# Performance work log

Measured on AMD Instinct MI355X. Metric: run time of the kernel, lower is better.

The kernel has to match this reference:

```python
import jax, jax.numpy as jnp
import numpy as np

COMMITMENT_COST = 0.25


def setup_inputs() -> dict:
    key = jax.random.key(0)
    k1, k2 = jax.random.split(key)
    inputs = jax.random.normal(k1, (32, 64, 64, 64), dtype=jnp.float32)  # b c h w
    num_embeddings, embedding_dim = 1024, 64
    # matches torch uniform_(-1/K, 1/K) init distributionally
    embedding = jax.random.uniform(
        k2, (num_embeddings, embedding_dim), dtype=jnp.float32,
        minval=-1.0 / num_embeddings, maxval=1.0 / num_embeddings)
    return {"inputs": inputs, "embedding": embedding}


def reference(inputs, embedding):
    # b c h w -> b h w c
    x = jnp.transpose(inputs, (0, 2, 3, 1))
    b, h, w, c = x.shape
    flat = x.reshape(-1, c)  # [N, D]
    dists = (jnp.sum(flat * flat, axis=1, keepdims=True)
             + jnp.sum(embedding * embedding, axis=1)
             - 2.0 * flat @ embedding.T)  # [N, K]
    idx = jnp.argmin(dists, axis=1)  # [N]
    quantized = embedding[idx].reshape(b, h, w, c)  # gather == one-hot matmul
    # elementwise MSE losses (reduction='none'); stop-gradient mirrors .detach()
    e_latent = (jax.lax.stop_gradient(quantized) - x) ** 2
    q_latent = (quantized - jax.lax.stop_gradient(x)) ** 2
    loss = q_latent + COMMITMENT_COST * e_latent  # [b, h, w, c]
    # straight-through estimator
    quantized_st = x + jax.lax.stop_gradient(quantized - x)
    quantized_out = jnp.transpose(quantized_st, (0, 3, 1, 2))  # b h w c -> b c h w
    return quantized_out, loss, idx.reshape(b, h, w)
```

## Files before the change

kernel.cpp:

```cpp
#include <hip/hip_runtime.h>

#define NPTS    131072
#define KC      1024
#define DD      64
#define HWSZ    4096
#define MARGINF 6e-5f
#define SLACKF  4e-5f

typedef __attribute__((ext_vector_type(8))) short short8;
typedef __attribute__((ext_vector_type(4))) float f32x4;

__device__ __forceinline__ ushort bf16_rne(float x) {
    unsigned u = __float_as_uint(x);
    unsigned r = u + 0x7fffu + ((u >> 16) & 1u);
    return (ushort)(r >> 16);
}

__device__ __forceinline__ float rdlane(float v, int d) {
    return __int_as_float(__builtin_amdgcn_readlane(__float_as_int(v), d));
}

__device__ __forceinline__ float exact_dv(float xrv, const float* __restrict__ emb,
                                          const float* __restrict__ se32,
                                          float sx, int k) {
    const float* er = emb + k * DD;
    double a = 0.0;
#pragma unroll 4
    for (int d = 0; d < DD; ++d)
        a = fma((double)rdlane(xrv, d), (double)er[d], a);
    float mm = (float)(2.0 * a);
    float s1, Dv;
    {
#pragma clang fp contract(off)
        s1 = sx + se32[k];
        Dv = s1 - mm;
    }
    return Dv;
}

__global__ void __launch_bounds__(256)
vq_prep_e(const float* __restrict__ emb, float* __restrict__ se32,
          float* __restrict__ sebB, ushort* __restrict__ Ebuf,
          float* __restrict__ embT, int* __restrict__ cnt) {
    __shared__ float es[16][68];
    const int tid  = threadIdx.x;
    const int tile = blockIdx.x;
    const int kbase = tile * 16;

    if (tile == 0 && tid == 0) *cnt = 0;

#pragma unroll
    for (int it = 0; it < 4; ++it) {
        int f = it * 256 + tid;
        es[f >> 6][f & 63] = emb[(size_t)kbase * DD + f];
    }
    __syncthreads();

    if (tid < 16) {
        float rr[8];
#pragma unroll
        for (int di = 0; di < 8; ++di) rr[di] = 0.0f;
        {
#pragma clang fp contract(off)
#pragma unroll
            for (int dm = 0; dm < 8; ++dm)
#pragma unroll
                for (int di = 0; di < 8; ++di) {
                    float ev = es[tid][dm * 8 + di];
                    rr[di] += ev * ev;
                }
        }
        float s;
        {
#pragma clang fp contract(off)
            s = ((rr[0] + rr[1]) + (rr[2] + rr[3])) + ((rr[4] + rr[5]) + (rr[6] + rr[7]));
        }
        se32[kbase + tid] = s;
        sebB[kbase + tid] = s + 0.5f;
    }

#pragma unroll
    for (int it = 0; it < 4; ++it) {
        int f = it * 256 + tid;
        int d = f >> 4, colk = f & 15;
        embT[d * KC + kbase + colk] = es[colk][d];
    }

#pragma unroll
    for (int it = 0; it < 8; ++it) {
        int f = it * 256 + tid;
        int sub = f >> 9;
        int pos = f & 511;
        int kh = sub >> 1, hl = sub & 1;
        int jj = pos & 7, colk = (pos >> 3) & 15, quad = pos >> 7;
        float ev = es[colk][kh * 32 + quad * 8 + jj];
        ushort hb = bf16_rne(ev);
        ushort val;
        if (hl == 0) {
            val = hb;
        } else {
            float hf = __uint_as_float(((unsigned)hb) << 16);
            val = bf16_rne(ev - hf);
        }
        Ebuf[((tile * 2 + kh) * 2 + hl) * 512 + pos] = val;
    }
}

__global__ void __launch_bounds__(256)
vq_main(const float* __restrict__ in, const float* __restrict__ emb,
        const ushort* __restrict__ Ebuf, const float* __restrict__ sebB,
        float* __restrict__ outq, float* __restrict__ outl, float* __restrict__ outi,
        int* __restrict__ cnt, int* __restrict__ queue) {
    __shared__ float xs[64][129];
    __shared__ int   sidx[128];
    const int tid = threadIdx.x;
    const int n0  = blockIdx.x * 128;
    const int b   = n0 >> 12;
    const int hw0 = n0 & 4095;
    const float* inb = in + (size_t)b * DD * HWSZ;

#pragma unroll
    for (int it = 0; it < 32; ++it) {
        int f = tid + it * 256;
        int c = f >> 7, j = f & 127;
        xs[c][j] = inb[c * HWSZ + hw0 + j];
    }
    __syncthreads();

    const int lane = tid & 63, wave = tid >> 6;
    const int quad = lane >> 4, col = lane & 15;

    short8 A[2][2][2];
#pragma unroll
    for (int p = 0; p < 2; ++p) {
        int pt = wave * 32 + p * 16 + col;
#pragma unroll
        for (int kh = 0; kh < 2; ++kh) {
            short8 ah, al;
#pragma unroll
            for (int j = 0; j < 8; ++j) {
                float xv = xs[kh * 32 + quad * 8 + j][pt];
                ushort hb = bf16_rne(xv);
                float  hf = __uint_as_float(((unsigned)hb) << 16);
                ah[j] = (short)hb;
                al[j] = (short)bf16_rne(xv - hf);
            }
            A[p][kh][0] = ah; A[p][kh][1] = al;
        }
    }

    unsigned b1[8], b2[8];
#pragma unroll
    for (int s = 0; s < 8; ++s) { b1[s] = 0xFFFFFFFFu; b2[s] = 0xFFFFFFFFu; }

    for (int g = 0; g < 16; ++g) {
        short8 B[4][2][2];
        float  sB[4];
#pragma unroll
        for (int s = 0; s < 4; ++s) {
            int tile = g * 4 + s;
            sB[s] = sebB[tile * 16 + col];
#pragma unroll
            for (int kh = 0; kh < 2; ++kh)
#pragma unroll
                for (int hl = 0; hl < 2; ++hl)
                    B[s][kh][hl] = *(const short8*)(Ebuf + ((tile * 2 + kh) * 2 + hl) * 512 + lane * 8);
        }
        f32x4 acc[2][4];
#pragma unroll
        for (int p = 0; p < 2; ++p)
#pragma unroll
            for (int s = 0; s < 4; ++s) acc[p][s] = (f32x4){0.f, 0.f, 0.f, 0.f};
#pragma unroll
        for (int p = 0; p < 2; ++p)
#pragma unroll
            for (int s = 0; s < 4; ++s) {
                acc[p][s] = __builtin_amdgcn_mfma_f32_16x16x32_bf16(A[p][0][0], B[s][0][0], acc[p][s], 0, 0, 0);
                acc[p][s] = __builtin_amdgcn_mfma_f32_16x16x32_bf16(A[p][1][0], B[s][1][0], acc[p][s], 0, 0, 0);
                acc[p][s] = __builtin_amdgcn_mfma_f32_16x16x32_bf16(A[p][0][0], B[s][0][1], acc[p][s], 0, 0, 0);
                acc[p][s] = __builtin_amdgcn_mfma_f32_16x16x32_bf16(A[p][1][0], B[s][1][1], acc[p][s], 0, 0, 0);
                acc[p][s] = __builtin_amdgcn_mfma_f32_16x16x32_bf16(A[p][0][1], B[s][0][0], acc[p][s], 0, 0, 0);
                acc[p][s] = __builtin_amdgcn_mfma_f32_16x16x32_bf16(A[p][1][1], B[s][1][0], acc[p][s], 0, 0, 0);
            }
#pragma unroll
        for (int p = 0; p < 2; ++p)
#pragma unroll
            for (int r = 0; r < 4; ++r) {
                unsigned q[4];
#pragma unroll
                for (int s = 0; s < 4; ++s) {
                    float t = fmaf(-2.f, acc[p][s][r], sB[s]);
                    q[s] = (__float_as_uint(t) & 0xFFFFFFC0u) | (unsigned)(g * 4 + s);
                }
                unsigned a  = min(q[0], q[1]), bb = max(q[0], q[1]);
                unsigned c2 = min(q[2], q[3]), d2 = max(q[2], q[3]);
                unsigned lo = min(a, c2), hi = max(a, c2);
                unsigned sec = min(min(bb, d2), hi);
                int sl = p * 4 + r;
                b2[sl] = min(min(b2[sl], sec), max(b1[sl], lo));
                b1[sl] = min(b1[sl], lo);
            }
    }

    unsigned v1[8], v2[8]; int ci[8];
#pragma unroll
    for (int s = 0; s < 8; ++s) {
        ci[s] = (int)(b1[s] & 63u) * 16 + col;
        v1[s] = b1[s] & 0xFFFFFFC0u;
        v2[s] = b2[s] & 0xFFFFFFC0u;
    }
#pragma unroll
    for (int off = 1; off < 16; off <<= 1) {
#pragma unroll
        for (int s = 0; s < 8; ++s) {
            unsigned o1 = (unsigned)__shfl_xor((int)v1[s], off);
            unsigned o2 = (unsigned)__shfl_xor((int)v2[s], off);
            int      oi = __shfl_xor(ci[s], off);
            unsigned nb2 = min(min(v2[s], o2), max(v1[s], o1));
            bool take = (o1 < v1[s]) || (o1 == v1[s] && oi < ci[s]);
            v1[s] = take ? o1 : v1[s];
            ci[s] = take ? oi : ci[s];
            v2[s] = nb2;
        }
    }
#pragma unroll
    for (int s = 0; s < 8; ++s) {
        if (col == s) {
            int jloc = wave * 32 + (s >> 2) * 16 + quad * 4 + (s & 3);
            sidx[jloc] = ci[s];
            float f1 = __uint_as_float(v1[s]), f2 = __uint_as_float(v2[s]);
            if (f2 - f1 < MARGINF) { int pos = atomicAdd(cnt, 1); queue[pos] = n0 + jloc; }
        }
    }
    __syncthreads();

    for (int t = 0; t < 32; ++t) {
        int jloc = wave * 32 + t;
        int kidx = sidx[jloc];
        float qv = emb[kidx * DD + lane];
        float x  = xs[lane][jloc];
        float dv = qv - x;
        float l  = dv * dv;
        outl[(size_t)(n0 + jloc) * DD + lane] = fmaf(0.25f, l, l);
        outq[((size_t)(b * DD) + lane) * HWSZ + hw0 + jloc] = x + (qv - x);
    }
    if (lane < 32) outi[n0 + wave * 32 + lane] = (float)sidx[wave * 32 + lane];
}

__global__ void __launch_bounds__(256)
vq_fix(const float* __restrict__ in, const float* __restrict__ emb,
       const float* __restrict__ embT, const float* __restrict__ se32,
       const int* __restrict__ queue, const int* __restrict__ cnt,
       float* __restrict__ outq, float* __restrict__ outl, float* __restrict__ outi) {
    const int lane = threadIdx.x & 63;
    const int gw   = blockIdx.x * 4 + (threadIdx.x >> 6);
    const int nwav = gridDim.x * 4;
    const int total = *cnt;
    for (int q0 = gw * 4; q0 < total; q0 += nwav * 4) {
        int   nn[4]; bool vld[4];
        float xr[4], sx4[4];
#pragma unroll
        for (int i = 0; i < 4; ++i) {
            int qi = q0 + i;
            vld[i] = (qi < total);
            nn[i]  = queue[vld[i] ? qi : q0];
            int b = nn[i] >> 12, hw = nn[i] & 4095;
            xr[i] = in[(size_t)b * DD * HWSZ + (size_t)lane * HWSZ + hw];
        }
#pragma unroll
        for (int i = 0; i < 4; ++i) {
            float rr[8];
#pragma unroll
            for (int di = 0; di < 8; ++di) rr[di] = 0.0f;
            for (int dm = 0; dm < 8; ++dm) {
#pragma unroll
                for (int di = 0; di < 8; ++di) {
                    float xv = rdlane(xr[i], dm * 8 + di);
                    {
#pragma clang fp contract(off)
                        rr[di] += xv * xv;
                    }
                }
            }
            {
#pragma clang fp contract(off)
                sx4[i] = ((rr[0] + rr[1]) + (rr[2] + rr[3])) + ((rr[4] + rr[5]) + (rr[6] + rr[7]));
            }
        }

        float m1[4], m2[4], m3[4]; int i1[4], i2[4];
#pragma unroll
        for (int i = 0; i < 4; ++i) {
            m1[i] = 3.4e38f; m2[i] = 3.4e38f; m3[i] = 3.4e38f;
            i1[i] = 0x7fffffff; i2[i] = 0x7fffffff;
        }

        for (int pass = 0; pass < 4; ++pass) {
            float acc[16];
#pragma unroll
            for (int a = 0; a < 16; ++a) acc[a] = 0.0f;
            const float* rpb = embT + (lane << 4) + pass * 4;
            for (int dm = 0; dm < 8; ++dm) {
#pragma unroll
                for (int di = 0; di < 8; ++di) {
                    const int d = dm * 8 + di;
                    f32x4 ev = *(const f32x4*)(rpb + (size_t)d * KC);
#pragma unroll
                    for (int i = 0; i < 4; ++i) {
                        float xv = rdlane(xr[i], d);
                        acc[i * 4 + 0] = fmaf(xv, ev[0], acc[i * 4 + 0]);
                        acc[i * 4 + 1] = fmaf(xv, ev[1], acc[i * 4 + 1]);
                        acc[i * 4 + 2] = fmaf(xv, ev[2], acc[i * 4 + 2]);
                        acc[i * 4 + 3] = fmaf(xv, ev[3], acc[i * 4 + 3]);
                    }
                }
            }
#pragma unroll
            for (int j = 0; j < 4; ++j) {
                int k = (lane << 4) + pass * 4 + j;
                float sek = se32[k];
#pragma unroll
                for (int i = 0; i < 4; ++i) {
                    float s = (sx4[i] + sek) - 2.0f * acc[i * 4 + j];
                    if (s < m1[i]) {
                        m3[i] = m2[i]; m2[i] = m1[i]; i2[i] = i1[i];
                        m1[i] = s; i1[i] = k;
                    } else if (s < m2[i]) {
                        m3[i] = m2[i]; m2[i] = s; i2[i] = k;
                    } else if (s < m3[i]) {
                        m3[i] = s;
                    }
                }
            }
        }

#pragma unroll
        for (int i = 0; i < 4; ++i) {
            float gm = m1[i];
#pragma unroll
            for (int off = 1; off < 64; off <<= 1)
                gm = fminf(gm, __shfl_xor(gm, off));
            const float thr = gm + SLACKF;

            float bD = 3.4e38f; int bi = 0x7fffffff;
            if (m3[i] <= thr) {
#pragma unroll 1
                for (int c = 0; c < 16; ++c) {
                    const int k = (lane << 4) + c;
                    float Dv = exact_dv(xr[i], emb, se32, sx4[i], k);
                    if (Dv < bD || (Dv == bD && k < bi)) { bD = Dv; bi = k; }
                }
            } else {
                if (m1[i] <= thr) {
                    const int k = i1[i];
                    float Dv = exact_dv(xr[i], emb, se32, sx4[i], k);
                    if (Dv < bD || (Dv == bD && k < bi)) { bD = Dv; bi = k; }
                }
                if (m2[i] <= thr) {
                    const int k = i2[i];
                    float Dv = exact_dv(xr[i], emb, se32, sx4[i], k);
                    if (Dv < bD || (Dv == bD && k < bi)) { bD = Dv; bi = k; }
                }
            }
#pragma unroll
            for (int off = 32; off > 0; off >>= 1) {
                float oD = __shfl_down(bD, off);
                int   oi = __shfl_down(bi, off);
                if (oD < bD || (oD == bD && oi < bi)) { bD = oD; bi = oi; }
            }
            bi = __shfl(bi, 0);
            if (vld[i]) {
                int n = nn[i];
                int old = (int)outi[n];
                if (bi != old) {
                    int bb = n >> 12, hw = n & 4095;
                    float xv = xr[i];
                    float qv = emb[bi * DD + lane];
                    float dv = qv - xv;
                    float l  = dv * dv;
                    outl[(size_t)n * DD + lane] = fmaf(0.25f, l, l);
                    outq[((size_t)bb * DD + lane) * HWSZ + hw] = xv + (qv - xv);
                    if (lane == 0) outi[n] = (float)bi;
                }
            }
        }
    }
}

extern "C" void kernel_launch(void* const* d_in, const int* in_sizes, int n_in,
                              void* d_out, int out_size, void* d_ws, size_t ws_size,
                              hipStream_t stream) {
    const float* in  = (const float*)d_in[0];
    const float* emb = (const float*)d_in[1];

    float* outq = (float*)d_out;
    float* outl = outq + (size_t)NPTS * DD;
    float* outi = outl + (size_t)NPTS * DD;

    char*   ws    = (char*)d_ws;
    float*  se32  = (float*)ws;
    float*  sebB  = (float*)(ws + 4096);
    ushort* Ebuf  = (ushort*)(ws + 8192);
    float*  embT  = (float*)(ws + 8192 + 262144);
    int*    cnt   = (int*)(ws + 8192 + 262144 + 262144);
    int*    queue = (int*)(ws + 8192 + 262144 + 262144 + 256);

    vq_prep_e<<<64, 256, 0, stream>>>(emb, se32, sebB, Ebuf, embT, cnt);
    vq_main<<<NPTS / 128, 256, 0, stream>>>(in, emb, Ebuf, sebB, outq, outl, outi, cnt, queue);
    vq_fix<<<2048, 256, 0, stream>>>(in, emb, embT, se32, queue, cnt, outq, outl, outi);
}
```

Baseline: 215.3 us.

## Fuse ambiguous-point fixup pass into main kernel using shared-memory queue

```diff
diff --git a/kernel.cpp b/kernel.cpp
--- a/kernel.cpp
+++ b/kernel.cpp
@@ -16,38 +16,14 @@
     return (ushort)(r >> 16);
 }
 
-__device__ __forceinline__ float rdlane(float v, int d) {
-    return __int_as_float(__builtin_amdgcn_readlane(__float_as_int(v), d));
-}
-
-__device__ __forceinline__ float exact_dv(float xrv, const float* __restrict__ emb,
-                                          const float* __restrict__ se32,
-                                          float sx, int k) {
-    const float* er = emb + k * DD;
-    double a = 0.0;
-#pragma unroll 4
-    for (int d = 0; d < DD; ++d)
-        a = fma((double)rdlane(xrv, d), (double)er[d], a);
-    float mm = (float)(2.0 * a);
-    float s1, Dv;
-    {
-#pragma clang fp contract(off)
-        s1 = sx + se32[k];
-        Dv = s1 - mm;
-    }
-    return Dv;
-}
-
 __global__ void __launch_bounds__(256)
 vq_prep_e(const float* __restrict__ emb, float* __restrict__ se32,
           float* __restrict__ sebB, ushort* __restrict__ Ebuf,
-          float* __restrict__ embT, int* __restrict__ cnt) {
+          float* __restrict__ embT) {
     __shared__ float es[16][68];
     const int tid  = threadIdx.x;
     const int tile = blockIdx.x;
     const int kbase = tile * 16;
-
-    if (tile == 0 && tid == 0) *cnt = 0;
 
 #pragma unroll
     for (int it = 0; it < 4; ++it) {
@@ -109,15 +85,19 @@
 __global__ void __launch_bounds__(256)
 vq_main(const float* __restrict__ in, const float* __restrict__ emb,
         const ushort* __restrict__ Ebuf, const float* __restrict__ sebB,
-        float* __restrict__ outq, float* __restrict__ outl, float* __restrict__ outi,
-        int* __restrict__ cnt, int* __restrict__ queue) {
+        const float* __restrict__ se32, const float* __restrict__ embT,
+        float* __restrict__ outq, float* __restrict__ outl, float* __restrict__ outi) {
     __shared__ float xs[64][129];
     __shared__ int   sidx[128];
+    __shared__ int   ambList[128];
+    __shared__ int   ambCnt;
     const int tid = threadIdx.x;
     const int n0  = blockIdx.x * 128;
     const int b   = n0 >> 12;
     const int hw0 = n0 & 4095;
     const float* inb = in + (size_t)b * DD * HWSZ;
+
+    if (tid == 0) ambCnt = 0;
 
 #pragma unroll
     for (int it = 0; it < 32; ++it) {
@@ -229,7 +209,7 @@
             int jloc = wave * 32 + (s >> 2) * 16 + quad * 4 + (s & 3);
             sidx[jloc] = ci[s];
             float f1 = __uint_as_float(v1[s]), f2 = __uint_as_float(v2[s]);
-            if (f2 - f1 < MARGINF) { int pos = atomicAdd(cnt, 1); queue[pos] = n0 + jloc; }
+            if (f2 - f1 < MARGINF) { int p = atomicAdd(&ambCnt, 1); ambList[p] = jloc; }
         }
     }
     __syncthreads();
@@ -245,28 +225,16 @@
         outq[((size_t)(b * DD) + lane) * HWSZ + hw0 + jloc] = x + (qv - x);
     }
     if (lane < 32) outi[n0 + wave * 32 + lane] = (float)sidx[wave * 32 + lane];
-}
-
-__global__ void __launch_bounds__(256)
-vq_fix(const float* __restrict__ in, const float* __restrict__ emb,
-       const float* __restrict__ embT, const float* __restrict__ se32,
-       const int* __restrict__ queue, const int* __restrict__ cnt,
-       float* __restrict__ outq, float* __restrict__ outl, float* __restrict__ outi) {
-    const int lane = threadIdx.x & 63;
-    const int gw   = blockIdx.x * 4 + (threadIdx.x >> 6);
-    const int nwav = gridDim.x * 4;
-    const int total = *cnt;
-    for (int q0 = gw * 4; q0 < total; q0 += nwav * 4) {
-        int   nn[4]; bool vld[4];
-        float xr[4], sx4[4];
-#pragma unroll
-        for (int i = 0; i < 4; ++i) {
-            int qi = q0 + i;
-            vld[i] = (qi < total);
-            nn[i]  = queue[vld[i] ? qi : q0];
-            int b = nn[i] >> 12, hw = nn[i] & 4095;
-            xr[i] = in[(size_t)b * DD * HWSZ + (size_t)lane * HWSZ + hw];
-        }
+    __syncthreads();
+
+    const int namb = ambCnt;
+    for (int base = wave * 4; base < namb; base += 16) {
+        const int cnt4 = (namb - base < 4) ? (namb - base) : 4;
+        int jl[4];
+#pragma unroll
+        for (int i = 0; i < 4; ++i) jl[i] = ambList[base + ((i < cnt4) ? i : 0)];
+
+        float sx4[4];
 #pragma unroll
         for (int i = 0; i < 4; ++i) {
             float rr[8];
@@ -275,7 +243,7 @@
             for (int dm = 0; dm < 8; ++dm) {
 #pragma unroll
                 for (int di = 0; di < 8; ++di) {
-                    float xv = rdlane(xr[i], dm * 8 + di);
+                    float xv = xs[dm * 8 + di][jl[i]];
                     {
 #pragma clang fp contract(off)
                         rr[di] += xv * xv;
@@ -307,7 +275,7 @@
                     f32x4 ev = *(const f32x4*)(rpb + (size_t)d * KC);
 #pragma unroll
                     for (int i = 0; i < 4; ++i) {
-                        float xv = rdlane(xr[i], d);
+                        float xv = xs[d][jl[i]];
                         acc[i * 4 + 0] = fmaf(xv, ev[0], acc[i * 4 + 0]);
                         acc[i * 4 + 1] = fmaf(xv, ev[1], acc[i * 4 + 1]);
                         acc[i * 4 + 2] = fmaf(xv, ev[2], acc[i * 4 + 2]);
@@ -341,24 +309,58 @@
             for (int off = 1; off < 64; off <<= 1)
                 gm = fminf(gm, __shfl_xor(gm, off));
             const float thr = gm + SLACKF;
+            const int jloc = jl[i];
 
             float bD = 3.4e38f; int bi = 0x7fffffff;
             if (m3[i] <= thr) {
 #pragma unroll 1
                 for (int c = 0; c < 16; ++c) {
                     const int k = (lane << 4) + c;
-                    float Dv = exact_dv(xr[i], emb, se32, sx4[i], k);
+                    const float* er = emb + k * DD;
+                    double a = 0.0;
+#pragma unroll 4
+                    for (int d = 0; d < DD; ++d)
+                        a = fma((double)xs[d][jloc], (double)er[d], a);
+                    float mm = (float)(2.0 * a);
+                    float s1, Dv;
+                    {
+#pragma clang fp contract(off)
+                        s1 = sx4[i] + se32[k];
+                        Dv = s1 - mm;
+                    }
                     if (Dv < bD || (Dv == bD && k < bi)) { bD = Dv; bi = k; }
                 }
             } else {
                 if (m1[i] <= thr) {
                     const int k = i1[i];
-                    float Dv = exact_dv(xr[i], emb, se32, sx4[i], k);
+                    const float* er = emb + k * DD;
+                    double a = 0.0;
+#pragma unroll 4
+                    for (int d = 0; d < DD; ++d)
+                        a = fma((double)xs[d][jloc], (double)er[d], a);
+                    float mm = (float)(2.0 * a);
+                    float s1, Dv;
+                    {
+#pragma clang fp contract(off)
+                        s1 = sx4[i] + se32[k];
+                        Dv = s1 - mm;
+                    }
                     if (Dv < bD || (Dv == bD && k < bi)) { bD = Dv; bi = k; }
                 }
                 if (m2[i] <= thr) {
                     const int k = i2[i];
-                    float Dv = exact_dv(xr[i], emb, se32, sx4[i], k);
+                    const float* er = emb + k * DD;
+                    double a = 0.0;
+#pragma unroll 4
+                    for (int d = 0; d < DD; ++d)
+                        a = fma((double)xs[d][jloc], (double)er[d], a);
+                    float mm = (float)(2.0 * a);
+                    float s1, Dv;
+                    {
+#pragma clang fp contract(off)
+                        s1 = sx4[i] + se32[k];
+                        Dv = s1 - mm;
+                    }
                     if (Dv < bD || (Dv == bD && k < bi)) { bD = Dv; bi = k; }
                 }
             }
@@ -369,19 +371,14 @@
                 if (oD < bD || (oD == bD && oi < bi)) { bD = oD; bi = oi; }
             }
             bi = __shfl(bi, 0);
-            if (vld[i]) {
-                int n = nn[i];
-                int old = (int)outi[n];
-                if (bi != old) {
-                    int bb = n >> 12, hw = n & 4095;
-                    float xv = xr[i];
-                    float qv = emb[bi * DD + lane];
-                    float dv = qv - xv;
-                    float l  = dv * dv;
-                    outl[(size_t)n * DD + lane] = fmaf(0.25f, l, l);
-                    outq[((size_t)bb * DD + lane) * HWSZ + hw] = xv + (qv - xv);
-                    if (lane == 0) outi[n] = (float)bi;
-                }
+            if (i < cnt4 && bi != sidx[jloc]) {
+                float x  = xs[lane][jloc];
+                float qv = emb[bi * DD + lane];
+                float dv = qv - x;
+                float l  = dv * dv;
+                outl[(size_t)(n0 + jloc) * DD + lane] = fmaf(0.25f, l, l);
+                outq[((size_t)(b * DD) + lane) * HWSZ + hw0 + jloc] = x + (qv - x);
+                if (lane == 0) outi[n0 + jloc] = (float)bi;
             }
         }
     }
@@ -402,10 +399,8 @@
     float*  sebB  = (float*)(ws + 4096);
     ushort* Ebuf  = (ushort*)(ws + 8192);
     float*  embT  = (float*)(ws + 8192 + 262144);
-    int*    cnt   = (int*)(ws + 8192 + 262144 + 262144);
-    int*    queue = (int*)(ws + 8192 + 262144 + 262144 + 256);
-
-    vq_prep_e<<<64, 256, 0, stream>>>(emb, se32, sebB, Ebuf, embT, cnt);
-    vq_main<<<NPTS / 128, 256, 0, stream>>>(in, emb, Ebuf, sebB, outq, outl, outi, cnt, queue);
-    vq_fix<<<2048, 256, 0, stream>>>(in, emb, embT, se32, queue, cnt, outq, outl, outi);
+
+    vq_prep_e<<<64, 256, 0, stream>>>(emb, se32, sebB, Ebuf, embT);
+    vq_main<<<NPTS / 128, 256, 0, stream>>>(in, emb, Ebuf, sebB, se32, embT,
+                                            outq, outl, outi);
 }
```

After: 316.5 us. 47.0% more time.
